# Optimization experiments

Measured on AMD Instinct MI355X. Metric: run time of the kernel, lower is better.

Reference implementation:

```python
import jax, jax.numpy as jnp
import numpy as np

B, T, K = 256, 1024, 128


def setup_inputs() -> dict:
    key = jax.random.key(0)
    k1, k2, k3, k4, k5 = jax.random.split(key, 5)
    EMISSIONS = jax.random.normal(k1, (B, T, K), dtype=jnp.float32)
    TAGS = jax.random.randint(k2, (B, T), 0, K, dtype=jnp.int64)
    MASK = jnp.ones((B, T), dtype=bool)
    START = jax.random.normal(k3, (K,), dtype=jnp.float32) * 0.01
    END = jax.random.normal(k4, (K,), dtype=jnp.float32) * 0.01
    TRANS = jax.random.normal(k5, (K, K), dtype=jnp.float32) * 0.01
    return {"EMISSIONS": EMISSIONS, "TAGS": TAGS, "MASK": MASK,
            "START": START, "END": END, "TRANS": TRANS}


def _forward_logz(emissions, mask, start, end, trans):
    # emissions (B,T,K), mask (B,T) bool -> logZ (B,)
    alpha0 = start[None, :] + emissions[:, 0, :]  # (B,K)

    def step(alpha, inp):
        emit, m = inp  # emit (B,K), m (B,) bool
        # PACK[b,i,j] = alpha[b,i] + trans[i,j]; logsumexp over prev tag i
        new = jax.nn.logsumexp(alpha[:, :, None] + trans[None, :, :], axis=1) + emit
        alpha = jnp.where(m[:, None], new, alpha)
        return alpha, None

    xs = (jnp.swapaxes(emissions[:, 1:, :], 0, 1),  # (T-1,B,K)
          jnp.swapaxes(mask[:, 1:], 0, 1))          # (T-1,B)
    alphaT, _ = jax.lax.scan(step, alpha0, xs)
    return jax.nn.logsumexp(alphaT + end[None, :], axis=1)


def _gold_score(emissions, tags, mask, start, end, trans):
    b = emissions.shape[0]
    ba = jnp.arange(b)
    maskf = mask.astype(emissions.dtype)
    sc0 = (start[tags[:, 0]] + emissions[ba, 0, tags[:, 0]]) * maskf[:, 0]
    pr = jnp.maximum(tags[:, :-1], 0)  # clamp(min=0)
    cr = jnp.maximum(tags[:, 1:], 0)
    m = (mask[:, 1:] & mask[:, :-1]).astype(emissions.dtype)  # (B,T-1)
    trans_sc = trans[pr, cr]  # (B,T-1)
    emit_sc = jnp.take_along_axis(emissions[:, 1:, :], cr[:, :, None], axis=2)[:, :, 0]
    sc = sc0 + jnp.sum((trans_sc + emit_sc) * m, axis=1)
    lenm1 = jnp.sum(mask.astype(jnp.int32), axis=1) - 1
    last = tags[ba, lenm1]
    return sc + end[last]


def reference(EMISSIONS, TAGS, MASK, START, END, TRANS):
    logz = _forward_logz(EMISSIONS, MASK, START, END, TRANS)
    gold = _gold_score(EMISSIONS, TAGS, MASK, START, END, TRANS)
    return jnp.mean(logz - gold)
```

## Files before the change

### kernel.cpp

```cpp
#include <hip/hip_runtime.h>
#include <math.h>

#define Bn 256
#define Tn 1024
#define Kn 128
#define NT 512
#define CH 16
#define CHF (CH * Kn)
#define CSTR 20
#define UW (8 * CSTR)
#define UIDX(j) (((j) >> 4) * CSTR + ((j) & 15))

__device__ __forceinline__ float red8(float s) {
    int t;
    t = __builtin_amdgcn_mov_dpp(__float_as_int(s), 0xB1, 0xF, 0xF, true);
    s += __int_as_float(t);
    t = __builtin_amdgcn_mov_dpp(__float_as_int(s), 0x4E, 0xF, 0xF, true);
    s += __int_as_float(t);
    t = __builtin_amdgcn_mov_dpp(__float_as_int(s), 0x128, 0xF, 0xF, true);
    s += __int_as_float(t);
    return s;
}

__global__ __launch_bounds__(NT, 2) void crf_fwd_kernel(
    const float* __restrict__ emis,
    const int*   __restrict__ tags,
    const float* __restrict__ startv,
    const float* __restrict__ endv,
    const float* __restrict__ trans,
    float* __restrict__ per_b)
{
    const int b    = blockIdx.x;
    const int tid  = threadIdx.x;
    const int wave = tid >> 6;
    const int lane = tid & 63;
    const int row16 = lane >> 4;
    const int rg    = (lane >> 2) & 1;
    const int p     = (lane & 3) | (((lane >> 3) & 1) << 2);
    const int c0    = wave * 16 + row16 * 4 + rg * 2;
    const bool wr   = ((lane & 0x0B) == 0);
    const int wslot = UIDX(c0);
    const int ubase = CSTR * p;

    __shared__ __align__(16) float U[2 * UW];
    __shared__ __align__(16) float Xs[2 * CHF];
    __shared__ float red[NT];

    const float* eb = emis + (size_t)b * Tn * Kn;
    const int*   tb = tags + b * Tn;

    const float* tp = trans + (size_t)(16 * p) * Kn + c0;
    float4 F0, F1, F2, F3, F4, F5, F6, F7;
#define LDE(k, Fk)                                                  \
    {                                                               \
        float2 ea = *(const float2*)(tp + (size_t)(2 * k) * Kn);    \
        float2 ec = *(const float2*)(tp + (size_t)(2 * k + 1) * Kn);\
        Fk = make_float4(__expf(ea.x), __expf(ea.y),                \
                         __expf(ec.x), __expf(ec.y));               \
    }
    LDE(0, F0) LDE(1, F1) LDE(2, F2) LDE(3, F3)
    LDE(4, F4) LDE(5, F5) LDE(6, F6) LDE(7, F7)
#undef LDE

    float gl = 0.f;
    for (int t = 1 + tid; t < Tn; t += NT) {
        int pt = tb[t - 1];
        int ct = tb[t];
        gl += trans[pt * Kn + ct] + eb[(size_t)t * Kn + ct];
    }
    if (tid == 0) {
        int t0 = tb[0];
        gl += startv[t0] + eb[t0] + endv[tb[Tn - 1]];
    }
    red[tid] = gl;

    {
        const float4* e4 = (const float4*)(eb + Kn);
        float4 a = e4[tid];
        ((float4*)Xs)[tid] =
            make_float4(__expf(a.x), __expf(a.y), __expf(a.z), __expf(a.w));
    }
    if (tid < Kn) {
        U[UW + UIDX(tid)] = __expf(startv[tid] + eb[tid]);
    }
    __syncthreads();

#pragma unroll
    for (int s = NT / 2; s > 0; s >>= 1) {
        if (tid < s) red[tid] += red[tid + s];
        __syncthreads();
    }
    const float gold = red[0];

    float  base = 0.f;
    float4 pf0  = make_float4(0, 0, 0, 0);

#define DOT2(qa, qb, Fk)                       \
    sa0 = fmaf(qa, Fk.x, sa0);                 \
    sa1 = fmaf(qa, Fk.y, sa1);                 \
    sb0 = fmaf(qb, Fk.z, sb0);                 \
    sb1 = fmaf(qb, Fk.w, sb1);

#define STEP(RB, SLOT, NORM)                                               \
    {                                                                      \
        const float4* Up4 = (const float4*)&U[(RB) * UW + ubase];          \
        float4 q0 = Up4[0], q1 = Up4[1], q2 = Up4[2], q3 = Up4[3];         \
        float2 xr = *(const float2*)&Xc[(SLOT) * Kn + c0];                 \
        float u0 = 0.f, rn = 0.f;                                          \
        if (NORM) { u0 = U[(RB) * UW]; rn = __builtin_amdgcn_rcpf(u0); }   \
        float sa0 = 0.f, sa1 = 0.f, sb0 = 0.f, sb1 = 0.f;                  \
        DOT2(q0.x, q0.y, F0) DOT2(q0.z, q0.w, F1)                          \
        DOT2(q1.x, q1.y, F2) DOT2(q1.z, q1.w, F3)                          \
        DOT2(q2.x, q2.y, F4) DOT2(q2.z, q2.w, F5)                          \
        DOT2(q3.x, q3.y, F6) DOT2(q3.z, q3.w, F7)                          \
        float m0 = (sa0 + sb0) * xr.x;                                     \
        float m1 = (sa1 + sb1) * xr.y;                                     \
        if (NORM) { m0 *= rn; m1 *= rn; base += __logf(u0); }              \
        float s0 = red8(m0);                                               \
        float s1 = red8(m1);                                               \
        if (wr) *(float2*)&U[((RB) ^ 1) * UW + wslot] = make_float2(s0, s1);\
        asm volatile("s_waitcnt lgkmcnt(0)" ::: "memory");                 \
        __builtin_amdgcn_s_barrier();                                      \
    }

    for (int cc = 0; cc < 63; ++cc) {
        const float* Xc = Xs + (cc & 1) * CHF;
        float*       Xn = (float*)Xs + ((cc & 1) ^ 1) * CHF;

        {
            const size_t base_el = (size_t)(16 * cc + 17) * Kn;
            const float4* s4 = (const float4*)(eb + base_el);
            pf0 = (base_el + (size_t)tid * 4 + 3 < (size_t)Tn * Kn)
                      ? s4[tid] : make_float4(0, 0, 0, 0);
        }

        STEP(1, 0,  true ) STEP(0, 1,  false) STEP(1, 2,  false) STEP(0, 3,  false)
        STEP(1, 4,  true ) STEP(0, 5,  false) STEP(1, 6,  false) STEP(0, 7,  false)

        ((float4*)Xn)[tid] =
            make_float4(__expf(pf0.x), __expf(pf0.y), __expf(pf0.z), __expf(pf0.w));

        STEP(1, 8,  true ) STEP(0, 9,  false) STEP(1, 10, false) STEP(0, 11, false)
        STEP(1, 12, true ) STEP(0, 13, false) STEP(1, 14, false) STEP(0, 15, false)
    }
    {
        const float* Xc = Xs + CHF;
        STEP(1, 0,  true ) STEP(0, 1,  false) STEP(1, 2,  false) STEP(0, 3,  false)
        STEP(1, 4,  true ) STEP(0, 5,  false) STEP(1, 6,  false) STEP(0, 7,  false)
        STEP(1, 8,  true ) STEP(0, 9,  false) STEP(1, 10, false) STEP(0, 11, false)
        STEP(1, 12, true ) STEP(0, 13, false) STEP(1, 14, false)
    }
#undef STEP
#undef DOT2

    float v = 0.f;
    if (tid < Kn) {
        float uT = U[UIDX(tid)];
        v = uT * __expf(endv[tid]);
    }
    red[tid] = v;
    __syncthreads();
#pragma unroll
    for (int s = NT / 2; s > 0; s >>= 1) {
        if (tid < s) red[tid] += red[tid + s];
        __syncthreads();
    }
    if (tid == 0)
        per_b[b] = base + __logf(red[0]) - gold;
}

__global__ __launch_bounds__(256) void crf_reduce(const float* __restrict__ per_b,
                                                  float* __restrict__ out) {
    __shared__ float red[256];
    int tid = threadIdx.x;
    red[tid] = per_b[tid];
    __syncthreads();
#pragma unroll
    for (int s = 128; s > 0; s >>= 1) {
        if (tid < s) red[tid] += red[tid + s];
        __syncthreads();
    }
    if (tid == 0) out[0] = red[0] * (1.0f / Bn);
}

extern "C" void kernel_launch(void* const* d_in, const int* in_sizes, int n_in,
                              void* d_out, int out_size, void* d_ws, size_t ws_size,
                              hipStream_t stream) {
    const float* emis   = (const float*)d_in[0];
    const int*   tags   = (const int*)d_in[1];
    const float* startv = (const float*)d_in[3];
    const float* endv   = (const float*)d_in[4];
    const float* trans  = (const float*)d_in[5];

    float* per_b = (float*)d_ws;

    crf_fwd_kernel<<<dim3(Bn), dim3(NT), 0, stream>>>(emis, tags, startv, endv,
                                                      trans, per_b);
    crf_reduce<<<dim3(1), dim3(256), 0, stream>>>(per_b, (float*)d_out);
}
```

Before: 457.2 us.

## Halve block size to 4 waves, each lane covering 32 predecessor tags

Reduces the CRF forward recursion block from 512 to 256 threads (4 waves). Each lane now holds 16 float4 of exp(trans) and reduces over 32 predecessor states, so the cross-lane DPP reduction drops from 3 stages to 2. The U buffer layout changes to 4 rows with stride 36, and each thread now prefetches two float4 of emissions per chunk. The aim is cheaper per-step barriers across fewer waves and a shorter shuffle chain on the serial critical path. The cost is more FMAs and LDS reads per lane, higher register pressure, and launch bounds set to 1 block per CU.

```diff
diff --git a/kernel.cpp b/kernel.cpp
--- a/kernel.cpp
+++ b/kernel.cpp
@@ -4,25 +4,14 @@
 #define Bn 256
 #define Tn 1024
 #define Kn 128
-#define NT 512
+#define NT 256
 #define CH 16
 #define CHF (CH * Kn)
-#define CSTR 20
-#define UW (8 * CSTR)
-#define UIDX(j) (((j) >> 4) * CSTR + ((j) & 15))
-
-__device__ __forceinline__ float red8(float s) {
-    int t;
-    t = __builtin_amdgcn_mov_dpp(__float_as_int(s), 0xB1, 0xF, 0xF, true);
-    s += __int_as_float(t);
-    t = __builtin_amdgcn_mov_dpp(__float_as_int(s), 0x4E, 0xF, 0xF, true);
-    s += __int_as_float(t);
-    t = __builtin_amdgcn_mov_dpp(__float_as_int(s), 0x128, 0xF, 0xF, true);
-    s += __int_as_float(t);
-    return s;
-}
-
-__global__ __launch_bounds__(NT, 2) void crf_fwd_kernel(
+#define USTR 36
+#define UW (4 * USTR)
+#define UIDX(j) (((j) >> 5) * USTR + ((j) & 31))
+
+__global__ __launch_bounds__(NT, 1) void crf_fwd_kernel(
     const float* __restrict__ emis,
     const int*   __restrict__ tags,
     const float* __restrict__ startv,
@@ -34,13 +23,12 @@
     const int tid  = threadIdx.x;
     const int wave = tid >> 6;
     const int lane = tid & 63;
-    const int row16 = lane >> 4;
-    const int rg    = (lane >> 2) & 1;
-    const int p     = (lane & 3) | (((lane >> 3) & 1) << 2);
-    const int c0    = wave * 16 + row16 * 4 + rg * 2;
-    const bool wr   = ((lane & 0x0B) == 0);
-    const int wslot = UIDX(c0);
-    const int ubase = CSTR * p;
+    const int g4   = lane >> 2;
+    const int q    = lane & 3;
+    const int c0   = wave * 32 + g4 * 2;
+    const bool wrt = (q == 0);
+    const int wslot = wave * USTR + 2 * g4;
+    const int ubase = q * USTR;
 
     __shared__ __align__(16) float U[2 * UW];
     __shared__ __align__(16) float Xs[2 * CHF];
@@ -49,8 +37,8 @@
     const float* eb = emis + (size_t)b * Tn * Kn;
     const int*   tb = tags + b * Tn;
 
-    const float* tp = trans + (size_t)(16 * p) * Kn + c0;
-    float4 F0, F1, F2, F3, F4, F5, F6, F7;
+    const float* tp = trans + (size_t)(32 * q) * Kn + c0;
+    float4 F0, F1, F2, F3, F4, F5, F6, F7, F8, F9, F10, F11, F12, F13, F14, F15;
 #define LDE(k, Fk)                                                  \
     {                                                               \
         float2 ea = *(const float2*)(tp + (size_t)(2 * k) * Kn);    \
@@ -58,8 +46,10 @@
         Fk = make_float4(__expf(ea.x), __expf(ea.y),                \
                          __expf(ec.x), __expf(ec.y));               \
     }
-    LDE(0, F0) LDE(1, F1) LDE(2, F2) LDE(3, F3)
-    LDE(4, F4) LDE(5, F5) LDE(6, F6) LDE(7, F7)
+    LDE(0, F0)   LDE(1, F1)   LDE(2, F2)   LDE(3, F3)
+    LDE(4, F4)   LDE(5, F5)   LDE(6, F6)   LDE(7, F7)
+    LDE(8, F8)   LDE(9, F9)   LDE(10, F10) LDE(11, F11)
+    LDE(12, F12) LDE(13, F13) LDE(14, F14) LDE(15, F15)
 #undef LDE
 
     float gl = 0.f;
@@ -77,8 +67,11 @@
     {
         const float4* e4 = (const float4*)(eb + Kn);
         float4 a = e4[tid];
+        float4 d = e4[tid + NT];
         ((float4*)Xs)[tid] =
             make_float4(__expf(a.x), __expf(a.y), __expf(a.z), __expf(a.w));
+        ((float4*)Xs)[tid + NT] =
+            make_float4(__expf(d.x), __expf(d.y), __expf(d.z), __expf(d.w));
     }
     if (tid < Kn) {
         U[UW + UIDX(tid)] = __expf(startv[tid] + eb[tid]);
@@ -94,31 +87,50 @@
 
     float  base = 0.f;
     float4 pf0  = make_float4(0, 0, 0, 0);
-
-#define DOT2(qa, qb, Fk)                       \
-    sa0 = fmaf(qa, Fk.x, sa0);                 \
-    sa1 = fmaf(qa, Fk.y, sa1);                 \
-    sb0 = fmaf(qb, Fk.z, sb0);                 \
-    sb1 = fmaf(qb, Fk.w, sb1);
+    float4 pf1  = make_float4(0, 0, 0, 0);
+
+#define DOT2A(qa, qb, Fk)                      \
+    aa0 = fmaf(qa, Fk.x, aa0);                 \
+    aa1 = fmaf(qa, Fk.y, aa1);                 \
+    ab0 = fmaf(qb, Fk.z, ab0);                 \
+    ab1 = fmaf(qb, Fk.w, ab1);
+#define DOT2B(qa, qb, Fk)                      \
+    ba0 = fmaf(qa, Fk.x, ba0);                 \
+    ba1 = fmaf(qa, Fk.y, ba1);                 \
+    bb0 = fmaf(qb, Fk.z, bb0);                 \
+    bb1 = fmaf(qb, Fk.w, bb1);
 
 #define STEP(RB, SLOT, NORM)                                               \
     {                                                                      \
         const float4* Up4 = (const float4*)&U[(RB) * UW + ubase];          \
-        float4 q0 = Up4[0], q1 = Up4[1], q2 = Up4[2], q3 = Up4[3];         \
+        float4 v0 = Up4[0], v1 = Up4[1], v2 = Up4[2], v3 = Up4[3];         \
+        float4 v4 = Up4[4], v5 = Up4[5], v6 = Up4[6], v7 = Up4[7];         \
         float2 xr = *(const float2*)&Xc[(SLOT) * Kn + c0];                 \
         float u0 = 0.f, rn = 0.f;                                          \
         if (NORM) { u0 = U[(RB) * UW]; rn = __builtin_amdgcn_rcpf(u0); }   \
-        float sa0 = 0.f, sa1 = 0.f, sb0 = 0.f, sb1 = 0.f;                  \
-        DOT2(q0.x, q0.y, F0) DOT2(q0.z, q0.w, F1)                          \
-        DOT2(q1.x, q1.y, F2) DOT2(q1.z, q1.w, F3)                          \
-        DOT2(q2.x, q2.y, F4) DOT2(q2.z, q2.w, F5)                          \
-        DOT2(q3.x, q3.y, F6) DOT2(q3.z, q3.w, F7)                          \
-        float m0 = (sa0 + sb0) * xr.x;                                     \
-        float m1 = (sa1 + sb1) * xr.y;                                     \
+        float aa0 = 0.f, aa1 = 0.f, ab0 = 0.f, ab1 = 0.f;                  \
+        float ba0 = 0.f, ba1 = 0.f, bb0 = 0.f, bb1 = 0.f;                  \
+        DOT2A(v0.x, v0.y, F0)  DOT2A(v0.z, v0.w, F1)                       \
+        DOT2A(v1.x, v1.y, F2)  DOT2A(v1.z, v1.w, F3)                       \
+        DOT2A(v2.x, v2.y, F4)  DOT2A(v2.z, v2.w, F5)                       \
+        DOT2A(v3.x, v3.y, F6)  DOT2A(v3.z, v3.w, F7)                       \
+        DOT2B(v4.x, v4.y, F8)  DOT2B(v4.z, v4.w, F9)                       \
+        DOT2B(v5.x, v5.y, F10) DOT2B(v5.z, v5.w, F11)                      \
+        DOT2B(v6.x, v6.y, F12) DOT2B(v6.z, v6.w, F13)                      \
+        DOT2B(v7.x, v7.y, F14) DOT2B(v7.z, v7.w, F15)                      \
+        float m0 = ((aa0 + ab0) + (ba0 + bb0)) * xr.x;                     \
+        float m1 = ((aa1 + ab1) + (ba1 + bb1)) * xr.y;                     \
         if (NORM) { m0 *= rn; m1 *= rn; base += __logf(u0); }              \
-        float s0 = red8(m0);                                               \
-        float s1 = red8(m1);                                               \
-        if (wr) *(float2*)&U[((RB) ^ 1) * UW + wslot] = make_float2(s0, s1);\
+        int t_;                                                            \
+        t_ = __builtin_amdgcn_mov_dpp(__float_as_int(m0), 0xB1, 0xF, 0xF, true); \
+        m0 += __int_as_float(t_);                                          \
+        t_ = __builtin_amdgcn_mov_dpp(__float_as_int(m1), 0xB1, 0xF, 0xF, true); \
+        m1 += __int_as_float(t_);                                          \
+        t_ = __builtin_amdgcn_mov_dpp(__float_as_int(m0), 0x4E, 0xF, 0xF, true); \
+        m0 += __int_as_float(t_);                                          \
+        t_ = __builtin_amdgcn_mov_dpp(__float_as_int(m1), 0x4E, 0xF, 0xF, true); \
+        m1 += __int_as_float(t_);                                          \
+        if (wrt) *(float2*)&U[((RB) ^ 1) * UW + wslot] = make_float2(m0, m1); \
         asm volatile("s_waitcnt lgkmcnt(0)" ::: "memory");                 \
         __builtin_amdgcn_s_barrier();                                      \
     }
@@ -132,6 +144,8 @@
             const float4* s4 = (const float4*)(eb + base_el);
             pf0 = (base_el + (size_t)tid * 4 + 3 < (size_t)Tn * Kn)
                       ? s4[tid] : make_float4(0, 0, 0, 0);
+            pf1 = (base_el + (size_t)(tid + NT) * 4 + 3 < (size_t)Tn * Kn)
+                      ? s4[tid + NT] : make_float4(0, 0, 0, 0);
         }
 
         STEP(1, 0,  true ) STEP(0, 1,  false) STEP(1, 2,  false) STEP(0, 3,  false)
@@ -139,6 +153,8 @@
 
         ((float4*)Xn)[tid] =
             make_float4(__expf(pf0.x), __expf(pf0.y), __expf(pf0.z), __expf(pf0.w));
+        ((float4*)Xn)[tid + NT] =
+            make_float4(__expf(pf1.x), __expf(pf1.y), __expf(pf1.z), __expf(pf1.w));
 
         STEP(1, 8,  true ) STEP(0, 9,  false) STEP(1, 10, false) STEP(0, 11, false)
         STEP(1, 12, true ) STEP(0, 13, false) STEP(1, 14, false) STEP(0, 15, false)
@@ -151,7 +167,8 @@
         STEP(1, 12, true ) STEP(0, 13, false) STEP(1, 14, false)
     }
 #undef STEP
-#undef DOT2
+#undef DOT2A
+#undef DOT2B
 
     float v = 0.f;
     if (tid < Kn) {
```

Measured after the change: 463.6 us. No clear change (+1.4%).
